# Performance work log

Measured on AMD Instinct MI355X. Metric: run time of the kernel, lower is better.

The kernel has to match this reference:

```python
import jax, jax.numpy as jnp
import numpy as np

GAMMA = 0.002  # init kwarg
N, M, D = 8192, 8192, 512


def setup_inputs() -> dict:
    key = jax.random.key(0)
    kx, ky = jax.random.split(key)
    x = jax.random.normal(kx, (N, D), dtype=jnp.float32)
    y = jax.random.normal(ky, (M, D), dtype=jnp.float32)
    return {"x": x, "y": y}


def reference(x, y):
    # k(x, y) = exp(-gamma * ||x - y||^2), using the GEMM identity
    x = x.reshape(-1, x.shape[-1])
    y = y.reshape(-1, y.shape[-1])
    x_sq = jnp.sum(x * x, axis=-1)          # [N]
    y_sq = jnp.sum(y * y, axis=-1)          # [M]
    xy = jnp.einsum('nd,md->nm', x, y)      # [N, M] GEMM
    sq_dist = x_sq[:, None] + y_sq[None, :] - 2.0 * xy
    sq_dist = jnp.maximum(sq_dist, 0.0)     # clamp fp cancellation
    return jnp.exp(-jnp.float32(GAMMA) * sq_dist)
```

## Files before the change

kernel.cpp:

```cpp
#include <hip/hip_runtime.h>
#include <hip/hip_bf16.h>

#define GAMMA 0.002f
#define NROWS 8192
#define MROWS 8192
#define DDIM  512

#define BM 256
#define BN 256
#define BK 64
#define KT (DDIM / BK)

typedef __attribute__((ext_vector_type(8))) short bf16x8;
typedef __attribute__((ext_vector_type(4))) float f32x4;
typedef __attribute__((ext_vector_type(8))) unsigned short ushort8;

static __device__ __forceinline__ unsigned short f32_to_bf16_rne(float f) {
    unsigned int u = __float_as_uint(f);
    unsigned int lsb = (u >> 16) & 1u;
    u += 0x7fffu + lsb;
    return (unsigned short)(u >> 16);
}

__global__ __launch_bounds__(64) void prep_kernel(const float* __restrict__ src,
                                                  unsigned short* __restrict__ dstb,
                                                  float* __restrict__ sq) {
    const int row  = blockIdx.x;
    const int lane = threadIdx.x;

    const float4* p = (const float4*)(src + (size_t)row * DDIM) + lane * 2;
    float4 f0 = p[0];
    float4 f1 = p[1];

    float s = f0.x*f0.x + f0.y*f0.y + f0.z*f0.z + f0.w*f0.w
            + f1.x*f1.x + f1.y*f1.y + f1.z*f1.z + f1.w*f1.w;

    float t[8] = {f0.x, f0.y, f0.z, f0.w, f1.x, f1.y, f1.z, f1.w};
    ushort8 hv;
#pragma unroll
    for (int i = 0; i < 8; ++i) hv[i] = f32_to_bf16_rne(t[i]);
    *(ushort8*)(dstb + (size_t)row * DDIM + lane * 8) = hv;

#pragma unroll
    for (int off = 32; off > 0; off >>= 1) s += __shfl_down(s, off);
    if (lane == 0) sq[row] = s;
}

__global__ __launch_bounds__(512, 2) void rbf_gemm_kernel(
        const unsigned short* __restrict__ xb,
        const unsigned short* __restrict__ yb,
        const float* __restrict__ xsq,
        const float* __restrict__ ysq,
        float* __restrict__ out) {
    __shared__ __align__(16) char smem[2 * 65536];

    const int tid  = threadIdx.x;
    const int wave = tid >> 6;
    const int lane = tid & 63;

    const int bid = (int)(blockIdx.y * gridDim.x + blockIdx.x);
    const int swz = (bid & 7) * 128 + (bid >> 3);
    const int rowBase = (swz & 31) * BM;
    const int colBase = (swz >> 5) * BN;

    const int wm = wave >> 2;
    const int wn = wave & 3;

    const int fr  = lane & 15;
    const int kb0 = ((lane >> 4) << 4) ^ ((lane & 7) << 4);
    const int kb1 = kb0 ^ 64;

    const int aoff = (wm * 128 + fr) * 128;
    const int boff = (wn * 64  + fr) * 128;

    const int srow8 = lane >> 3;
    const int sgsrc = ((lane & 7) ^ (lane >> 3)) << 4;
    const size_t arowg = (size_t)(rowBase + wave * 32 + srow8) * (DDIM * 2);
    const size_t browg = (size_t)(colBase + wave * 32 + srow8) * (DDIM * 2);
    const char* xg = (const char*)xb;
    const char* yg = (const char*)yb;
    char* sm = (char*)smem;

    f32x4 acc[8][4];
#pragma unroll
    for (int m = 0; m < 8; ++m)
#pragma unroll
        for (int n = 0; n < 4; ++n) acc[m][n] = (f32x4){0.f, 0.f, 0.f, 0.f};

    auto STAGE = [&](int kt, int c) {
        const int kb = kt * 128 + sgsrc;
#pragma unroll
        for (int s = 0; s < 4; ++s) {
            __builtin_amdgcn_global_load_lds(
                (__attribute__((address_space(1))) void*)(xg + arowg + (size_t)s * 8192 + kb),
                (__attribute__((address_space(3))) void*)(sm + c * 65536 + wave * 4096 + s * 1024),
                16, 0, 0);
            __builtin_amdgcn_global_load_lds(
                (__attribute__((address_space(1))) void*)(yg + browg + (size_t)s * 8192 + kb),
                (__attribute__((address_space(3))) void*)(sm + c * 65536 + 32768 + wave * 4096 + s * 1024),
                16, 0, 0);
        }
    };

    STAGE(0, 0);
    asm volatile("" ::: "memory");
    STAGE(1, 1);
    asm volatile("s_waitcnt vmcnt(8)" ::: "memory");
    __builtin_amdgcn_s_barrier();
    asm volatile("" ::: "memory");

#pragma unroll
    for (int t = 0; t < KT; ++t) {
        const int c = t & 1;
        const char* smc = sm + c * 65536;
        bf16x8 A0[8], B0[4], A1[8], B1[4];

#pragma unroll
        for (int m = 0; m < 8; ++m) A0[m] = *(const bf16x8*)(smc + aoff + m * 2048 + kb0);
#pragma unroll
        for (int n = 0; n < 4; ++n) B0[n] = *(const bf16x8*)(smc + 32768 + boff + n * 2048 + kb0);
        __builtin_amdgcn_s_setprio(1);
#pragma unroll
        for (int m = 0; m < 8; ++m)
#pragma unroll
            for (int n = 0; n < 4; ++n)
                acc[m][n] = __builtin_amdgcn_mfma_f32_16x16x32_bf16(A0[m], B0[n], acc[m][n], 0, 0, 0);
        __builtin_amdgcn_s_setprio(0);

#pragma unroll
        for (int m = 0; m < 8; ++m) A1[m] = *(const bf16x8*)(smc + aoff + m * 2048 + kb1);
#pragma unroll
        for (int n = 0; n < 4; ++n) B1[n] = *(const bf16x8*)(smc + 32768 + boff + n * 2048 + kb1);
        asm volatile("s_waitcnt lgkmcnt(0)" ::: "memory");
        __builtin_amdgcn_s_barrier();
        asm volatile("" ::: "memory");

        if (t + 2 < KT) STAGE(t + 2, c);

        __builtin_amdgcn_s_setprio(1);
#pragma unroll
        for (int m = 0; m < 8; ++m)
#pragma unroll
            for (int n = 0; n < 4; ++n)
                acc[m][n] = __builtin_amdgcn_mfma_f32_16x16x32_bf16(A1[m], B1[n], acc[m][n], 0, 0, 0);
        __builtin_amdgcn_s_setprio(0);

        if (t + 2 < KT)      { asm volatile("s_waitcnt vmcnt(8)" ::: "memory"); }
        else if (t + 1 < KT) { asm volatile("s_waitcnt vmcnt(0)" ::: "memory"); }
        __builtin_amdgcn_s_barrier();
        asm volatile("" ::: "memory");
    }

    const int q4 = (lane >> 4) * 4;
    const int rb = rowBase + wm * 128;
    const int cb = colBase + wn * 64;
#pragma unroll
    for (int m = 0; m < 8; ++m) {
        float xr[4];
#pragma unroll
        for (int r2 = 0; r2 < 4; ++r2) xr[r2] = xsq[rb + m * 16 + q4 + r2];
#pragma unroll
        for (int n = 0; n < 4; ++n) {
            const int gcol = cb + n * 16 + fr;
            const float ysq_c = ysq[gcol];
#pragma unroll
            for (int r2 = 0; r2 < 4; ++r2) {
                const int grow = rb + m * 16 + q4 + r2;
                float d = xr[r2] + ysq_c - 2.0f * acc[m][n][r2];
                d = fmaxf(d, 0.0f);
                out[(size_t)grow * MROWS + gcol] = __expf(-GAMMA * d);
            }
        }
    }
}

extern "C" void kernel_launch(void* const* d_in, const int* in_sizes, int n_in,
                              void* d_out, int out_size, void* d_ws, size_t ws_size,
                              hipStream_t stream) {
    const float* x = (const float*)d_in[0];
    const float* y = (const float*)d_in[1];
    float* out = (float*)d_out;

    unsigned short* xb = (unsigned short*)d_ws;
    unsigned short* yb = xb + (size_t)NROWS * DDIM;
    float* xsq = (float*)(yb + (size_t)MROWS * DDIM);
    float* ysq = xsq + NROWS;

    prep_kernel<<<NROWS, 64, 0, stream>>>(x, xb, xsq);
    prep_kernel<<<MROWS, 64, 0, stream>>>(y, yb, ysq);

    dim3 grid(NROWS / BM, MROWS / BN);
    rbf_gemm_kernel<<<grid, 512, 0, stream>>>(xb, yb, xsq, ysq, out);
}
```

Measured before the change: 389.9 us.

## Split K-loop into four sub-phases with finer-grained staggered LDS prefetch

Restructures the main loop so that each K-tile is processed in four quarter phases of 16 MFMAs each. Global-to-LDS loads are split into A-even, A-odd, B-first and B-second chunks, issued in different phases. The next tile's chunks are interleaved with the current compute, with vmcnt waits tuned per phase. The smaller operand register sets are meant to cut VGPR pressure and spread memory traffic more evenly against MFMA work. In exchange the loop has more barriers per tile and a more fragile ordering between the buffers and the wait counts.

Measured after the change: 387.1 us. Within noise of the previous version (-0.7%).

```diff
diff --git a/kernel.cpp b/kernel.cpp
--- a/kernel.cpp
+++ b/kernel.cpp
@@ -14,6 +14,13 @@
 typedef __attribute__((ext_vector_type(8))) short bf16x8;
 typedef __attribute__((ext_vector_type(4))) float f32x4;
 typedef __attribute__((ext_vector_type(8))) unsigned short ushort8;
+
+#define AS1 __attribute__((address_space(1)))
+#define AS3 __attribute__((address_space(3)))
+#define FENCE asm volatile("" ::: "memory")
+#define BARRIER do { FENCE; __builtin_amdgcn_s_barrier(); FENCE; } while (0)
+#define VMCNT(n) asm volatile("s_waitcnt vmcnt(" #n ")" ::: "memory")
+#define LGKM0    asm volatile("s_waitcnt lgkmcnt(0)" ::: "memory")
 
 static __device__ __forceinline__ unsigned short f32_to_bf16_rne(float f) {
     unsigned int u = __float_as_uint(f);
@@ -53,6 +60,7 @@
         const float* __restrict__ ysq,
         float* __restrict__ out) {
     __shared__ __align__(16) char smem[2 * 65536];
+    char* sm = (char*)smem;
 
     const int tid  = threadIdx.x;
     const int wave = tid >> 6;
@@ -69,17 +77,42 @@
     const int fr  = lane & 15;
     const int kb0 = ((lane >> 4) << 4) ^ ((lane & 7) << 4);
     const int kb1 = kb0 ^ 64;
-
     const int aoff = (wm * 128 + fr) * 128;
     const int boff = (wn * 64  + fr) * 128;
 
-    const int srow8 = lane >> 3;
-    const int sgsrc = ((lane & 7) ^ (lane >> 3)) << 4;
-    const size_t arowg = (size_t)(rowBase + wave * 32 + srow8) * (DDIM * 2);
-    const size_t browg = (size_t)(colBase + wave * 32 + srow8) * (DDIM * 2);
+    const int srow = tid >> 3;
+    const int skb  = (((tid & 7) ^ ((tid >> 3) & 7)) << 4);
     const char* xg = (const char*)xb;
     const char* yg = (const char*)yb;
-    char* sm = (char*)smem;
+
+    auto stg1 = [&](const char* g, int growBase, int kt, int ldsOff) {
+        __builtin_amdgcn_global_load_lds(
+            (AS1 void*)(g + (size_t)(growBase + srow) * (DDIM * 2) + kt * 128 + skb),
+            (AS3 void*)(sm + ldsOff + tid * 16), 16, 0, 0);
+    };
+    auto stAEV = [&](int kt, int c) {
+        stg1(xg, rowBase +   0, kt, c * 65536 +     0);
+        stg1(xg, rowBase + 128, kt, c * 65536 + 16384);
+    };
+    auto stAOD = [&](int kt, int c) {
+        stg1(xg, rowBase +  64, kt, c * 65536 +  8192);
+        stg1(xg, rowBase + 192, kt, c * 65536 + 24576);
+    };
+    auto stB1 = [&](int kt, int c) {
+        stg1(yg, colBase +   0, kt, c * 65536 + 32768);
+        stg1(yg, colBase +  64, kt, c * 65536 + 40960);
+    };
+    auto stB2 = [&](int kt, int c) {
+        stg1(yg, colBase + 128, kt, c * 65536 + 49152);
+        stg1(yg, colBase + 192, kt, c * 65536 + 57344);
+    };
+
+    auto ldA = [&](const char* smc, int m, int kb) -> bf16x8 {
+        return *(const bf16x8*)(smc + aoff + m * 2048 + kb);
+    };
+    auto ldB = [&](const char* smc, int n, int kb) -> bf16x8 {
+        return *(const bf16x8*)(smc + 32768 + boff + n * 2048 + kb);
+    };
 
     f32x4 acc[8][4];
 #pragma unroll
@@ -87,68 +120,72 @@
 #pragma unroll
         for (int n = 0; n < 4; ++n) acc[m][n] = (f32x4){0.f, 0.f, 0.f, 0.f};
 
-    auto STAGE = [&](int kt, int c) {
-        const int kb = kt * 128 + sgsrc;
-#pragma unroll
-        for (int s = 0; s < 4; ++s) {
-            __builtin_amdgcn_global_load_lds(
-                (__attribute__((address_space(1))) void*)(xg + arowg + (size_t)s * 8192 + kb),
-                (__attribute__((address_space(3))) void*)(sm + c * 65536 + wave * 4096 + s * 1024),
-                16, 0, 0);
-            __builtin_amdgcn_global_load_lds(
-                (__attribute__((address_space(1))) void*)(yg + browg + (size_t)s * 8192 + kb),
-                (__attribute__((address_space(3))) void*)(sm + c * 65536 + 32768 + wave * 4096 + s * 1024),
-                16, 0, 0);
-        }
-    };
-
-    STAGE(0, 0);
-    asm volatile("" ::: "memory");
-    STAGE(1, 1);
-    asm volatile("s_waitcnt vmcnt(8)" ::: "memory");
-    __builtin_amdgcn_s_barrier();
-    asm volatile("" ::: "memory");
+    stAEV(0, 0); stB1(0, 0); stB2(0, 0); stAOD(0, 0); stAEV(1, 1);
+    VMCNT(4);
+    BARRIER;
 
 #pragma unroll
     for (int t = 0; t < KT; ++t) {
         const int c = t & 1;
         const char* smc = sm + c * 65536;
-        bf16x8 A0[8], B0[4], A1[8], B1[4];
-
-#pragma unroll
-        for (int m = 0; m < 8; ++m) A0[m] = *(const bf16x8*)(smc + aoff + m * 2048 + kb0);
-#pragma unroll
-        for (int n = 0; n < 4; ++n) B0[n] = *(const bf16x8*)(smc + 32768 + boff + n * 2048 + kb0);
-        __builtin_amdgcn_s_setprio(1);
-#pragma unroll
-        for (int m = 0; m < 8; ++m)
-#pragma unroll
-            for (int n = 0; n < 4; ++n)
-                acc[m][n] = __builtin_amdgcn_mfma_f32_16x16x32_bf16(A0[m], B0[n], acc[m][n], 0, 0, 0);
-        __builtin_amdgcn_s_setprio(0);
-
-#pragma unroll
-        for (int m = 0; m < 8; ++m) A1[m] = *(const bf16x8*)(smc + aoff + m * 2048 + kb1);
-#pragma unroll
-        for (int n = 0; n < 4; ++n) B1[n] = *(const bf16x8*)(smc + 32768 + boff + n * 2048 + kb1);
-        asm volatile("s_waitcnt lgkmcnt(0)" ::: "memory");
-        __builtin_amdgcn_s_barrier();
-        asm volatile("" ::: "memory");
-
-        if (t + 2 < KT) STAGE(t + 2, c);
-
-        __builtin_amdgcn_s_setprio(1);
-#pragma unroll
-        for (int m = 0; m < 8; ++m)
-#pragma unroll
-            for (int n = 0; n < 4; ++n)
-                acc[m][n] = __builtin_amdgcn_mfma_f32_16x16x32_bf16(A1[m], B1[n], acc[m][n], 0, 0, 0);
-        __builtin_amdgcn_s_setprio(0);
-
-        if (t + 2 < KT)      { asm volatile("s_waitcnt vmcnt(8)" ::: "memory"); }
-        else if (t + 1 < KT) { asm volatile("s_waitcnt vmcnt(0)" ::: "memory"); }
-        __builtin_amdgcn_s_barrier();
-        asm volatile("" ::: "memory");
+        bf16x8 av[4], bv[4];
+
+        if (t + 1 < KT) stB1(t + 1, c ^ 1);
+#pragma unroll
+        for (int m = 0; m < 4; ++m) av[m] = ldA(smc, m, kb0);
+#pragma unroll
+        for (int n = 0; n < 4; ++n) bv[n] = ldB(smc, n, kb0);
+        __builtin_amdgcn_s_setprio(1);
+#pragma unroll
+        for (int m = 0; m < 4; ++m)
+#pragma unroll
+            for (int n = 0; n < 4; ++n)
+                acc[m][n] = __builtin_amdgcn_mfma_f32_16x16x32_bf16(av[m], bv[n], acc[m][n], 0, 0, 0);
+        __builtin_amdgcn_s_setprio(0);
+        if (t + 1 < KT) { VMCNT(4); } else { VMCNT(0); }
+        BARRIER;
+
+        if (t + 1 < KT) stB2(t + 1, c ^ 1);
+#pragma unroll
+        for (int m = 0; m < 4; ++m) av[m] = ldA(smc, 4 + m, kb0);
+        __builtin_amdgcn_s_setprio(1);
+#pragma unroll
+        for (int m = 0; m < 4; ++m)
+#pragma unroll
+            for (int n = 0; n < 4; ++n)
+                acc[4 + m][n] = __builtin_amdgcn_mfma_f32_16x16x32_bf16(av[m], bv[n], acc[4 + m][n], 0, 0, 0);
+        __builtin_amdgcn_s_setprio(0);
+        BARRIER;
+
+        if (t + 1 < KT) stAOD(t + 1, c ^ 1);
+#pragma unroll
+        for (int m = 0; m < 4; ++m) av[m] = ldA(smc, m, kb1);
+#pragma unroll
+        for (int n = 0; n < 4; ++n) bv[n] = ldB(smc, n, kb1);
+        __builtin_amdgcn_s_setprio(1);
+#pragma unroll
+        for (int m = 0; m < 4; ++m)
+#pragma unroll
+            for (int n = 0; n < 4; ++n)
+                acc[m][n] = __builtin_amdgcn_mfma_f32_16x16x32_bf16(av[m], bv[n], acc[m][n], 0, 0, 0);
+        __builtin_amdgcn_s_setprio(0);
+        LGKM0;
+        BARRIER;
+
+        if (t + 2 < KT) stAEV(t + 2, c);
+#pragma unroll
+        for (int m = 0; m < 4; ++m) av[m] = ldA(smc, 4 + m, kb1);
+        __builtin_amdgcn_s_setprio(1);
+#pragma unroll
+        for (int m = 0; m < 4; ++m)
+#pragma unroll
+            for (int n = 0; n < 4; ++n)
+                acc[4 + m][n] = __builtin_amdgcn_mfma_f32_16x16x32_bf16(av[m], bv[n], acc[4 + m][n], 0, 0, 0);
+        __builtin_amdgcn_s_setprio(0);
+        if (t + 2 < KT)      { VMCNT(4); }
+        else if (t + 1 < KT) { VMCNT(2); }
+        LGKM0;
+        if (t + 1 < KT) BARRIER;
     }
 
     const int q4 = (lane >> 4) * 4;
```
